# Performance work log

Measured on AMD Instinct MI355X. Metric: run time of the kernel, lower is better.

The kernel has to match this reference:

```python
import jax, jax.numpy as jnp
import numpy as np

E, HID, T, B, NH, DFF, A, C = 116, 64, 512, 64, 4, 2048, 116, 90


def _ln(x, g, b, eps=1e-5):
    m = x.mean(-1, keepdims=True)
    v = ((x - m) ** 2).mean(-1, keepdims=True)
    return (x - m) / jnp.sqrt(v + eps) * g + b


def _layer(x, p):
    # torch TransformerEncoderLayer, post-norm, relu, eval mode (no dropout)
    wqkv, bqkv, wo, bo, g1, bn1, w1, b1, w2, b2, g2, bn2 = p
    S, N, Em = x.shape  # note: S is the attended axis (dim 0), N the batched axis
    dh = Em // NH
    qkv = x @ wqkv.T + bqkv
    q, k, v = jnp.split(qkv, 3, axis=-1)
    q = q.reshape(S, N, NH, dh)
    k = k.reshape(S, N, NH, dh)
    v = v.reshape(S, N, NH, dh)
    scores = jnp.einsum('snhd,tnhd->nhst', q, k) / np.float32(np.sqrt(dh))
    attn = jax.nn.softmax(scores, axis=-1)
    o = jnp.einsum('nhst,tnhd->snhd', attn, v).reshape(S, N, Em)
    o = o @ wo.T + bo
    x = _ln(x + o, g1, bn1)
    f = jax.nn.relu(x @ w1.T + b1) @ w2.T + b2
    return _ln(x + f, g2, bn2)


def _forward(x, sim, p1, p2, fc_w, fc_b):
    out = _layer(x, p1)
    out1 = _layer(out, p2)
    outs = jnp.transpose(out1, (0, 2, 1))       # (B, E, T)
    fea_ = outs @ fc_w.T + fc_b                 # (B, E, HID)
    feas = jnp.transpose(fea_, (0, 2, 1))       # (B, HID, E)
    fea = feas[:, None, :, :, None]             # (B,1,HID,E,1)
    sim32 = sim.astype(jnp.float32)             # (A, HID, C)
    # cosine_similarity over the HID axis (dim=2 of broadcast tensors),
    # computed without materializing the (B,A,HID,E,C) broadcast product.
    dot = jnp.einsum('bhd,ahc->badc', feas, sim32)           # (B,A,E,C)
    fn = jnp.linalg.norm(feas, axis=1)                       # (B,E)
    sn = jnp.linalg.norm(sim32, axis=1)                      # (A,C)
    denom = jnp.maximum(fn[:, None, :, None] * sn[None, :, None, :], 1e-8)
    similarity = dot / denom                                 # (B,A,E,C)
    similar = similarity.reshape(-1, 116 * 90)
    nrm = jnp.maximum(jnp.linalg.norm(similar, axis=1, keepdims=True), 1e-12)
    similar = similar / nrm
    return fea, similarity, similar


_PNAMES = ['wqkv', 'bqkv', 'wo', 'bo', 'g1', 'bn1', 'w1', 'b1', 'w2', 'b2', 'g2', 'bn2']
_PSHAPES = [(3 * E, E), (3 * E,), (E, E), (E,), (E,), (E,), (DFF, E), (DFF,), (E, DFF), (E,), (E,), (E,)]


def setup_inputs() -> dict:
    key = jax.random.key(0)
    ks = jax.random.split(key, 32)
    s = 0.02
    inp = {
        'x': jax.random.normal(ks[0], (B, T, E), jnp.float32),
        'sim': jax.random.normal(ks[1], (A, HID, C), jnp.float32),
    }
    i = 2
    for L in ('l1', 'l2'):
        for nm, sh in zip(_PNAMES, _PSHAPES):
            if nm in ('g1', 'g2'):
                inp[f'{L}_{nm}'] = jnp.ones(sh, jnp.float32)
            elif nm in ('bqkv', 'bo', 'bn1', 'b1', 'b2', 'bn2'):
                inp[f'{L}_{nm}'] = jnp.zeros(sh, jnp.float32)
            else:
                inp[f'{L}_{nm}'] = jax.random.normal(ks[i], sh, jnp.float32) * s
                i += 1
    inp['fc_w'] = jax.random.normal(ks[i], (HID, T), jnp.float32) * s
    inp['fc_b'] = jnp.zeros((HID,), jnp.float32)
    return inp


def reference(x, sim,
              l1_wqkv, l1_bqkv, l1_wo, l1_bo, l1_g1, l1_bn1, l1_w1, l1_b1, l1_w2, l1_b2, l1_g2, l1_bn2,
              l2_wqkv, l2_bqkv, l2_wo, l2_bo, l2_g1, l2_bn1, l2_w1, l2_b1, l2_w2, l2_b2, l2_g2, l2_bn2,
              fc_w, fc_b):
    p1 = (l1_wqkv, l1_bqkv, l1_wo, l1_bo, l1_g1, l1_bn1, l1_w1, l1_b1, l1_w2, l1_b2, l1_g2, l1_bn2)
    p2 = (l2_wqkv, l2_bqkv, l2_wo, l2_bo, l2_g1, l2_bn1, l2_w1, l2_b1, l2_w2, l2_b2, l2_g2, l2_bn2)
    return _forward(x, sim, p1, p2, fc_w, fc_b)
```

## Files before the change

kernel.cpp:

```cpp
#include <hip/hip_runtime.h>
#include <hip/hip_bf16.h>

typedef __attribute__((ext_vector_type(8))) short short8v;
typedef __attribute__((ext_vector_type(4))) float floatx4;
typedef unsigned short ushort_t;

__device__ __forceinline__ float bf2f(unsigned short u) {
  union { unsigned int i; float f; } c;
  c.i = ((unsigned int)u) << 16;
  return c.f;
}
__device__ __forceinline__ unsigned short f2bf(float f) {
  __hip_bfloat16 h = __float2bfloat16(f);
  return *reinterpret_cast<unsigned short*>(&h);
}

struct ConvJobs {
  const float* src[9];
  unsigned short* dst[9];
  int K[9];
  int Kp[9];
  int mode[9];
  int cum[10];
};

__global__ __launch_bounds__(256) void convert_all_kernel(ConvJobs J) {
  const int total = J.cum[9];
  for (int idx = blockIdx.x * 256 + threadIdx.x; idx < total;
       idx += gridDim.x * 256) {
    int j = 0;
    while (idx >= J.cum[j + 1]) ++j;
    const int local = idx - J.cum[j];
    const int Kp = J.Kp[j];
    const int r = local / Kp, c = local - r * Kp;
    unsigned short v;
    if (J.mode[j] == 0) {
      v = (c < J.K[j]) ? f2bf(J.src[j][(size_t)r * J.K[j] + c])
                       : (unsigned short)0;
    } else {
      const int h = c >> 5, d = c & 31;
      v = (d < 29) ? f2bf(J.src[j][(size_t)r * 116 + h * 29 + d])
                   : (unsigned short)0;
    }
    J.dst[j][local] = v;
  }
}

template <int MODE>
__global__ __launch_bounds__(256) void mgemm_kernel(
    const unsigned short* __restrict__ A, const unsigned short* __restrict__ B,
    const float* __restrict__ bias, int N, int Kp, int ldout,
    unsigned short* __restrict__ Yb) {
  __shared__ __align__(16) unsigned short As[128][64];
  __shared__ __align__(16) unsigned short Bs[128][64];

  const int tid = threadIdx.x;
  const int M0 = blockIdx.x * 128;
  const int N0 = blockIdx.y * 128;
  const int wid = tid >> 6, lane = tid & 63;
  const int wr = wid >> 1, wc = wid & 1;
  const int lc = lane & 15, g = lane >> 4;
  const int srow = tid >> 1, shalf = tid & 1;
  const int sw = srow & 7;

  floatx4 acc[4][4] = {};

  const int nk = Kp >> 6;
  for (int kt = 0; kt < nk; ++kt) {
    const int k0 = kt << 6;
    {
      const uint4* p = reinterpret_cast<const uint4*>(
          A + (size_t)(M0 + srow) * Kp + k0 + shalf * 32);
      uint4 v0 = p[0], v1 = p[1], v2 = p[2], v3 = p[3];
      *reinterpret_cast<uint4*>(&As[srow][((((shalf << 2) | 0) ^ sw) << 3)]) = v0;
      *reinterpret_cast<uint4*>(&As[srow][((((shalf << 2) | 1) ^ sw) << 3)]) = v1;
      *reinterpret_cast<uint4*>(&As[srow][((((shalf << 2) | 2) ^ sw) << 3)]) = v2;
      *reinterpret_cast<uint4*>(&As[srow][((((shalf << 2) | 3) ^ sw) << 3)]) = v3;
    }
    {
      uint4 v0 = {0, 0, 0, 0}, v1 = v0, v2 = v0, v3 = v0;
      const int jr = N0 + srow;
      if (jr < N) {
        const uint4* p = reinterpret_cast<const uint4*>(
            B + (size_t)jr * Kp + k0 + shalf * 32);
        v0 = p[0]; v1 = p[1]; v2 = p[2]; v3 = p[3];
      }
      *reinterpret_cast<uint4*>(&Bs[srow][((((shalf << 2) | 0) ^ sw) << 3)]) = v0;
      *reinterpret_cast<uint4*>(&Bs[srow][((((shalf << 2) | 1) ^ sw) << 3)]) = v1;
      *reinterpret_cast<uint4*>(&Bs[srow][((((shalf << 2) | 2) ^ sw) << 3)]) = v2;
      *reinterpret_cast<uint4*>(&Bs[srow][((((shalf << 2) | 3) ^ sw) << 3)]) = v3;
    }
    __syncthreads();
#pragma unroll
    for (int ks = 0; ks < 2; ++ks) {
      short8v a[4], b[4];
#pragma unroll
      for (int m = 0; m < 4; ++m) {
        const int row = wr * 64 + m * 16 + lc;
        a[m] = *reinterpret_cast<const short8v*>(
            &As[row][((((ks << 2) | g) ^ (lc & 7)) << 3)]);
      }
#pragma unroll
      for (int n = 0; n < 4; ++n) {
        const int col = wc * 64 + n * 16 + lc;
        b[n] = *reinterpret_cast<const short8v*>(
            &Bs[col][((((ks << 2) | g) ^ (lc & 7)) << 3)]);
      }
#pragma unroll
      for (int m = 0; m < 4; ++m)
#pragma unroll
        for (int n = 0; n < 4; ++n)
          acc[m][n] = __builtin_amdgcn_mfma_f32_16x16x32_bf16(a[m], b[n],
                                                              acc[m][n], 0, 0, 0);
    }
    __syncthreads();
  }

#pragma unroll
  for (int m = 0; m < 4; ++m) {
#pragma unroll
    for (int r = 0; r < 4; ++r) {
      const int row = M0 + wr * 64 + m * 16 + g * 4 + r;
#pragma unroll
      for (int n = 0; n < 4; ++n) {
        const int col = N0 + wc * 64 + n * 16 + lc;
        if (col < N) {
          float v = acc[m][n][r] + bias[col];
          if (MODE == 1) v = fmaxf(v, 0.f);
          if constexpr (MODE == 3) {
            const int which = (col >= 232) ? 2 : (col >= 116 ? 1 : 0);
            const int cw = col - which * 116;
            const int h = (cw * 565) >> 14;
            const int d = cw - h * 29;
            const int nn2 = row & 511, ss = row >> 9;
            Yb[(size_t)which * 4194304 +
               ((((size_t)nn2 * 4 + h) * 64 + ss) << 5) + d] = f2bf(v);
          } else {
            Yb[(size_t)row * ldout + col] = f2bf(v);
          }
        }
      }
    }
  }
}

__global__ __launch_bounds__(256) void mgemm64_ln_kernel(
    const unsigned short* __restrict__ A, const unsigned short* __restrict__ B,
    const float* __restrict__ bias, int Kp, unsigned short* __restrict__ Yb,
    float* __restrict__ Yf, const float* __restrict__ res,
    const float* __restrict__ gw, const float* __restrict__ bw) {
  __shared__ __align__(16) unsigned short As[64][64];
  __shared__ __align__(16) unsigned short Bs[128][64];
  __shared__ float sum1[2][64];
  __shared__ float sum2[2][64];

  const int tid = threadIdx.x;
  const int M0 = blockIdx.x * 64;
  const int wid = tid >> 6, lane = tid & 63;
  const int wr = wid >> 1, wc = wid & 1;
  const int lc = lane & 15, g = lane >> 4;
  const int arow = tid >> 2, aq = tid & 3;
  const int brow = tid >> 1, bhalf = tid & 1;

  floatx4 acc[2][4] = {};

  const int nk = Kp >> 6;
  for (int kt = 0; kt < nk; ++kt) {
    const int k0 = kt << 6;
    {
      const uint4* p = reinterpret_cast<const uint4*>(
          A + (size_t)(M0 + arow) * Kp + k0 + aq * 16);
      uint4 v0 = p[0], v1 = p[1];
      const int swa = arow & 7;
      *reinterpret_cast<uint4*>(&As[arow][(((aq * 2) ^ swa) << 3)]) = v0;
      *reinterpret_cast<uint4*>(&As[arow][(((aq * 2 + 1) ^ swa) << 3)]) = v1;
    }
    {
      uint4 v0 = {0, 0, 0, 0}, v1 = v0, v2 = v0, v3 = v0;
      if (brow < 116) {
        const uint4* p = reinterpret_cast<const uint4*>(
            B + (size_t)brow * Kp + k0 + bhalf * 32);
        v0 = p[0]; v1 = p[1]; v2 = p[2]; v3 = p[3];
      }
      const int sw = brow & 7;
      *reinterpret_cast<uint4*>(&Bs[brow][((((bhalf << 2) | 0) ^ sw) << 3)]) = v0;
      *reinterpret_cast<uint4*>(&Bs[brow][((((bhalf << 2) | 1) ^ sw) << 3)]) = v1;
      *reinterpret_cast<uint4*>(&Bs[brow][((((bhalf << 2) | 2) ^ sw) << 3)]) = v2;
      *reinterpret_cast<uint4*>(&Bs[brow][((((bhalf << 2) | 3) ^ sw) << 3)]) = v3;
    }
    __syncthreads();
#pragma unroll
    for (int ks = 0; ks < 2; ++ks) {
      short8v a[2], b[4];
#pragma unroll
      for (int m = 0; m < 2; ++m) {
        const int row = wr * 32 + m * 16 + lc;
        a[m] = *reinterpret_cast<const short8v*>(
            &As[row][((((ks << 2) | g) ^ (row & 7)) << 3)]);
      }
#pragma unroll
      for (int n = 0; n < 4; ++n) {
        const int col = wc * 64 + n * 16 + lc;
        b[n] = *reinterpret_cast<const short8v*>(
            &Bs[col][((((ks << 2) | g) ^ (col & 7)) << 3)]);
      }
#pragma unroll
      for (int m = 0; m < 2; ++m)
#pragma unroll
        for (int n = 0; n < 4; ++n)
          acc[m][n] = __builtin_amdgcn_mfma_f32_16x16x32_bf16(a[m], b[n],
                                                              acc[m][n], 0, 0, 0);
    }
    __syncthreads();
  }

  float s1l[2][4], s2l[2][4];
#pragma unroll
  for (int m = 0; m < 2; ++m) {
#pragma unroll
    for (int r = 0; r < 4; ++r) {
      const int row = M0 + wr * 32 + m * 16 + g * 4 + r;
      float s = 0.f, s2 = 0.f;
#pragma unroll
      for (int n = 0; n < 4; ++n) {
        const int col = wc * 64 + n * 16 + lc;
        float v = 0.f;
        if (col < 116)
          v = acc[m][n][r] + bias[col] + res[(size_t)row * 116 + col];
        acc[m][n][r] = v;
        s += v;
        s2 = fmaf(v, v, s2);
      }
#pragma unroll
      for (int st = 1; st < 16; st <<= 1) {
        s += __shfl_xor(s, st, 16);
        s2 += __shfl_xor(s2, st, 16);
      }
      s1l[m][r] = s;
      s2l[m][r] = s2;
    }
  }
  if (lc == 0) {
#pragma unroll
    for (int m = 0; m < 2; ++m)
#pragma unroll
      for (int r = 0; r < 4; ++r) {
        const int lrow = wr * 32 + m * 16 + g * 4 + r;
        sum1[wc][lrow] = s1l[m][r];
        sum2[wc][lrow] = s2l[m][r];
      }
  }
  __syncthreads();
#pragma unroll
  for (int m = 0; m < 2; ++m) {
#pragma unroll
    for (int r = 0; r < 4; ++r) {
      const int lrow = wr * 32 + m * 16 + g * 4 + r;
      const int row = M0 + lrow;
      const float st = sum1[0][lrow] + sum1[1][lrow];
      const float s2t = sum2[0][lrow] + sum2[1][lrow];
      const float mean = st * (1.f / 116.f);
      const float var = s2t * (1.f / 116.f) - mean * mean;
      const float rstd = 1.f / sqrtf(var + 1e-5f);
#pragma unroll
      for (int n = 0; n < 4; ++n) {
        const int col = wc * 64 + n * 16 + lc;
        if (col < 116) {
          const float y = (acc[m][n][r] - mean) * rstd * gw[col] + bw[col];
          Yf[(size_t)row * 116 + col] = y;
          Yb[(size_t)row * 128 + col] = f2bf(y);
        } else {
          Yb[(size_t)row * 128 + col] = 0;
        }
      }
    }
  }
}

__global__ __launch_bounds__(64) void attn_kernel(
    const unsigned short* __restrict__ qkvp, unsigned short* __restrict__ obuf) {
  const int h = blockIdx.x & 3;
  const int n = blockIdx.x >> 2;
  const int s = threadIdx.x;
  __shared__ float ks[64][36];
  __shared__ float vs[64][36];

  const size_t rb = (((size_t)n * 4 + h) * 64 + s) * 32;
  const uint4* qp = reinterpret_cast<const uint4*>(qkvp + rb);
  const uint4* kp = reinterpret_cast<const uint4*>(qkvp + 4194304 + rb);
  const uint4* vp = reinterpret_cast<const uint4*>(qkvp + 8388608 + rb);
  uint4 qv[4], kv4[4], vv4[4];
#pragma unroll
  for (int i = 0; i < 4; ++i) {
    qv[i] = qp[i];
    kv4[i] = kp[i];
    vv4[i] = vp[i];
  }
  float q[32], kf[32], vf[32];
#pragma unroll
  for (int i = 0; i < 4; ++i) {
    const unsigned* wq = reinterpret_cast<const unsigned*>(&qv[i]);
    const unsigned* wk = reinterpret_cast<const unsigned*>(&kv4[i]);
    const unsigned* wv = reinterpret_cast<const unsigned*>(&vv4[i]);
#pragma unroll
    for (int j = 0; j < 4; ++j) {
      union { unsigned u; float f; } lo, hi;
      const int d0 = i * 8 + 2 * j;
      lo.u = wq[j] << 16; hi.u = wq[j] & 0xffff0000u;
      q[d0] = lo.f; q[d0 + 1] = hi.f;
      lo.u = wk[j] << 16; hi.u = wk[j] & 0xffff0000u;
      kf[d0] = (d0 < 29) ? lo.f : 0.f;
      kf[d0 + 1] = (d0 + 1 < 29) ? hi.f : 0.f;
      lo.u = wv[j] << 16; hi.u = wv[j] & 0xffff0000u;
      vf[d0] = (d0 < 29) ? lo.f : 0.f;
      vf[d0 + 1] = (d0 + 1 < 29) ? hi.f : 0.f;
    }
  }
  q[29] = q[30] = q[31] = 0.f;
#pragma unroll
  for (int c = 0; c < 8; ++c) {
    *reinterpret_cast<float4*>(&ks[s][c * 4]) =
        make_float4(kf[4 * c], kf[4 * c + 1], kf[4 * c + 2], kf[4 * c + 3]);
    *reinterpret_cast<float4*>(&vs[s][c * 4]) =
        make_float4(vf[4 * c], vf[4 * c + 1], vf[4 * c + 2], vf[4 * c + 3]);
  }
  __syncthreads();

  const float scale = 0.18569533817705186f;
  float sc[64];
#pragma unroll 4
  for (int t = 0; t < 64; ++t) {
    const float4* kr = reinterpret_cast<const float4*>(&ks[t][0]);
    float a = 0.f;
#pragma unroll
    for (int c = 0; c < 8; ++c) {
      const float4 kc = kr[c];
      a = fmaf(q[4 * c], kc.x, a);
      a = fmaf(q[4 * c + 1], kc.y, a);
      a = fmaf(q[4 * c + 2], kc.z, a);
      a = fmaf(q[4 * c + 3], kc.w, a);
    }
    sc[t] = a * scale;
  }
  float m = sc[0];
#pragma unroll
  for (int t = 1; t < 64; ++t) m = fmaxf(m, sc[t]);
  float sum = 0.f;
#pragma unroll
  for (int t = 0; t < 64; ++t) {
    sc[t] = __expf(sc[t] - m);
    sum += sc[t];
  }
  const float inv = 1.f / sum;
  float o[32] = {};
#pragma unroll 4
  for (int t = 0; t < 64; ++t) {
    const float p = sc[t];
    const float4* vr = reinterpret_cast<const float4*>(&vs[t][0]);
#pragma unroll
    for (int c = 0; c < 8; ++c) {
      const float4 vc = vr[c];
      o[4 * c] = fmaf(p, vc.x, o[4 * c]);
      o[4 * c + 1] = fmaf(p, vc.y, o[4 * c + 1]);
      o[4 * c + 2] = fmaf(p, vc.z, o[4 * c + 2]);
      o[4 * c + 3] = fmaf(p, vc.w, o[4 * c + 3]);
    }
  }
  unsigned short ow[32];
#pragma unroll
  for (int i = 0; i < 32; ++i) ow[i] = f2bf(o[i] * inv);
  uint4* od =
      reinterpret_cast<uint4*>(obuf + ((size_t)s * 512 + n) * 128 + h * 32);
  const uint4* ows = reinterpret_cast<const uint4*>(ow);
#pragma unroll
  for (int i = 0; i < 4; ++i) od[i] = ows[i];
}

__global__ __launch_bounds__(256) void fc_kernel(const float* __restrict__ X4,
                                                 const float* __restrict__ fw,
                                                 const float* __restrict__ fb,
                                                 float* __restrict__ fea) {
  const int eg = blockIdx.x;
  const int b = blockIdx.y;
  const int e0 = eg * 29;
  __shared__ float Os[64][30];
  __shared__ float Wf[64][65];
  const int tid = threadIdx.x;
  const int h = tid & 63, jg = tid >> 6;
  float acc[8] = {};

  for (int tc = 0; tc < 8; ++tc) {
    for (int idx = tid; idx < 64 * 29; idx += 256) {
      int tt = idx / 29;
      int ee = idx - tt * 29;
      Os[tt][ee] = X4[((size_t)b * 512 + tc * 64 + tt) * 116 + e0 + ee];
    }
    for (int idx = tid; idx < 64 * 64; idx += 256) {
      int hh = idx >> 6, t2 = idx & 63;
      Wf[hh][t2] = fw[(size_t)hh * 512 + tc * 64 + t2];
    }
    __syncthreads();
#pragma unroll 4
    for (int t = 0; t < 64; ++t) {
      const float w = Wf[h][t];
#pragma unroll
      for (int m = 0; m < 8; ++m) {
        const int el = jg + 4 * m;
        if (el < 29) acc[m] = fmaf(Os[t][el], w, acc[m]);
      }
    }
    __syncthreads();
  }
  const float bb = fb[h];
#pragma unroll
  for (int m = 0; m < 8; ++m) {
    const int el = jg + 4 * m;
    if (el < 29) fea[((size_t)b * 64 + h) * 116 + e0 + el] = acc[m] + bb;
  }
}

__global__ __launch_bounds__(256) void sim_prep_kernel(
    const float* __restrict__ fea, const float* __restrict__ simin,
    unsigned short* __restrict__ feaT, unsigned short* __restrict__ simT,
    float* __restrict__ fn, float* __restrict__ sn) {
  __shared__ float L[64][121];
  const int blk = blockIdx.x;
  const int tid = threadIdx.x;
  if (blk < 64) {
    const int b = blk;
    for (int idx = tid; idx < 64 * 116; idx += 256) {
      const int h = idx / 116, d = idx - h * 116;
      L[h][d] = bf2f(f2bf(fea[((size_t)b * 64 + h) * 116 + d]));
    }
    __syncthreads();
    for (int idx = tid; idx < 128 * 64; idx += 256) {
      const int d = idx >> 6, h = idx & 63;
      feaT[((size_t)b * 128 + d) * 64 + h] = (d < 116) ? f2bf(L[h][d]) : 0;
    }
    if (tid < 116) {
      float s = 0.f;
#pragma unroll 8
      for (int h = 0; h < 64; ++h) {
        const float t = L[h][tid];
        s = fmaf(t, t, s);
      }
      fn[b * 128 + tid] = sqrtf(s);
    }
  } else {
    const int a = blk - 64;
    for (int idx = tid; idx < 64 * 90; idx += 256) {
      const int h = idx / 90, c = idx - h * 90;
      L[h][c] = bf2f(f2bf(simin[((size_t)a * 64 + h) * 90 + c]));
    }
    __syncthreads();
    for (int idx = tid; idx < 96 * 64; idx += 256) {
      const int c = idx >> 6, h = idx & 63;
      simT[((size_t)a * 96 + c) * 64 + h] = (c < 90) ? f2bf(L[h][c]) : 0;
    }
    if (tid < 90) {
      float s = 0.f;
#pragma unroll 8
      for (int h = 0; h < 64; ++h) {
        const float t = L[h][tid];
        s = fmaf(t, t, s);
      }
      sn[a * 96 + tid] = sqrtf(s);
    }
  }
}

__global__ __launch_bounds__(256) void sim_mfma2_kernel(
    const unsigned short* __restrict__ feaT, const unsigned short* __restrict__ simT,
    const float* __restrict__ fn, const float* __restrict__ sn,
    float* __restrict__ simil, float* __restrict__ similar) {
  const int a = blockIdx.x;
  const int b = blockIdx.y;
  __shared__ __align__(16) unsigned char shmem[41760];
  __shared__ float fnrow[116];
  __shared__ float snrow[90];
  __shared__ float wred[4];
  const int tid = threadIdx.x;

  unsigned short (*Ft)[64] = reinterpret_cast<unsigned short(*)[64]>(shmem);
  unsigned short (*St)[64] =
      reinterpret_cast<unsigned short(*)[64]>(shmem + 16384);
  float* Rs = reinterpret_cast<float*>(shmem);

  const int srow = tid >> 1, shalf = tid & 1;
  const int sw = srow & 7;
  {
    const uint4* p = reinterpret_cast<const uint4*>(
        feaT + ((size_t)b * 128 + srow) * 64 + shalf * 32);
    uint4 v0 = p[0], v1 = p[1], v2 = p[2], v3 = p[3];
    *reinterpret_cast<uint4*>(&Ft[srow][((((shalf << 2) | 0) ^ sw) << 3)]) = v0;
    *reinterpret_cast<uint4*>(&Ft[srow][((((shalf << 2) | 1) ^ sw) << 3)]) = v1;
    *reinterpret_cast<uint4*>(&Ft[srow][((((shalf << 2) | 2) ^ sw) << 3)]) = v2;
    *reinterpret_cast<uint4*>(&Ft[srow][((((shalf << 2) | 3) ^ sw) << 3)]) = v3;
  }
  if (srow < 96) {
    const uint4* p = reinterpret_cast<const uint4*>(
        simT + ((size_t)a * 96 + srow) * 64 + shalf * 32);
    uint4 v0 = p[0], v1 = p[1], v2 = p[2], v3 = p[3];
    *reinterpret_cast<uint4*>(&St[srow][((((shalf << 2) | 0) ^ sw) << 3)]) = v0;
    *reinterpret_cast<uint4*>(&St[srow][((((shalf << 2) | 1) ^ sw) << 3)]) = v1;
    *reinterpret_cast<uint4*>(&St[srow][((((shalf << 2) | 2) ^ sw) << 3)]) = v2;
    *reinterpret_cast<uint4*>(&St[srow][((((shalf << 2) | 3) ^ sw) << 3)]) = v3;
  }
  if (tid < 116) fnrow[tid] = fn[b * 128 + tid];
  else if (tid >= 128 && tid < 218) snrow[tid - 128] = sn[a * 96 + tid - 128];
  __syncthreads();

  const int wid = tid >> 6, lane = tid & 63;
  const int wr = wid >> 1, wc = wid & 1;
  const int lc = lane & 15, g = lane >> 4;

  floatx4 acc[4][3] = {};
#pragma unroll
  for (int ks = 0; ks < 2; ++ks) {
    short8v av[4], bv[3];
#pragma unroll
    for (int m = 0; m < 4; ++m) {
      const int row = wr * 64 + m * 16 + lc;
      av[m] = *reinterpret_cast<const short8v*>(
          &Ft[row][((((ks << 2) | g) ^ (lc & 7)) << 3)]);
    }
#pragma unroll
    for (int n = 0; n < 3; ++n) {
      const int col = wc * 48 + n * 16 + lc;
      bv[n] = *reinterpret_cast<const short8v*>(
          &St[col][((((ks << 2) | g) ^ (lc & 7)) << 3)]);
    }
#pragma unroll
    for (int m = 0; m < 4; ++m)
#pragma unroll
      for (int n = 0; n < 3; ++n)
        acc[m][n] = __builtin_amdgcn_mfma_f32_16x16x32_bf16(av[m], bv[n],
                                                            acc[m][n], 0, 0, 0);
  }
  __syncthreads();

  float ss = 0.f;
#pragma unroll
  for (int m = 0; m < 4; ++m) {
#pragma unroll
    for (int r = 0; r < 4; ++r) {
      const int d = wr * 64 + m * 16 + g * 4 + r;
      if (d < 116) {
        const float fnv = fnrow[d];
#pragma unroll
        for (int n = 0; n < 3; ++n) {
          const int c = wc * 48 + n * 16 + lc;
          if (c < 90) {
            const float denom = fmaxf(fnv * snrow[c], 1e-8f);
            float rcp = __builtin_amdgcn_rcpf(denom);
            rcp = rcp * (2.0f - denom * rcp);
            const float v = acc[m][n][r] * rcp;
            ss = fmaf(v, v, ss);
            Rs[d * 90 + c] = v;
          }
        }
      }
    }
  }
#pragma unroll
  for (int st = 1; st <= 32; st <<= 1) ss += __shfl_xor(ss, st, 64);
  if (lane == 0) wred[wid] = ss;
  __syncthreads();
  const float tot = wred[0] + wred[1] + wred[2] + wred[3];
  const float inv = 1.f / fmaxf(sqrtf(tot), 1e-12f);

  const size_t rowbase = ((size_t)b * 116 + a) * (116 * 90);
  float4* so = reinterpret_cast<float4*>(simil + rowbase);
  float4* sr = reinterpret_cast<float4*>(similar + rowbase);
  const float4* rs4 = reinterpret_cast<const float4*>(Rs);
  for (int i = tid; i < 2610; i += 256) {
    float4 v = rs4[i];
    so[i] = v;
    float4 w;
    w.x = v.x * inv; w.y = v.y * inv; w.z = v.z * inv; w.w = v.w * inv;
    sr[i] = w;
  }
}

__global__ __launch_bounds__(256) void sim_mfma_kernel(
    const float* __restrict__ fea, const float* __restrict__ simin,
    float* __restrict__ simil, float* __restrict__ similar) {
  const int a = blockIdx.x;
  const int b = blockIdx.y;
  __shared__ __align__(16) unsigned char shmem[41760];
  __shared__ float fnrow[116];
  __shared__ float snrow[90];
  __shared__ float wred[4];
  const int tid = threadIdx.x;

  unsigned short (*Ft)[64] = reinterpret_cast<unsigned short(*)[64]>(shmem);
  unsigned short (*St)[64] =
      reinterpret_cast<unsigned short(*)[64]>(shmem + 16384);
  float* Rs = reinterpret_cast<float*>(shmem);

  for (int idx = tid; idx < 64 * 116; idx += 256) {
    const int h = idx / 116, d = idx - h * 116;
    Ft[d][(((h >> 3) ^ (d & 7)) << 3) | (h & 7)] =
        f2bf(fea[((size_t)b * 64 + h) * 116 + d]);
  }
  for (int idx = tid; idx < 12 * 64; idx += 256) {
    const int d = 116 + (idx >> 6), h = idx & 63;
    Ft[d][(((h >> 3) ^ (d & 7)) << 3) | (h & 7)] = 0;
  }
  for (int idx = tid; idx < 64 * 90; idx += 256) {
    const int h = idx / 90, c = idx - h * 90;
    St[c][(((h >> 3) ^ (c & 7)) << 3) | (h & 7)] =
        f2bf(simin[((size_t)a * 64 + h) * 90 + c]);
  }
  for (int idx = tid; idx < 6 * 64; idx += 256) {
    const int c = 90 + (idx >> 6), h = idx & 63;
    St[c][(((h >> 3) ^ (c & 7)) << 3) | (h & 7)] = 0;
  }
  __syncthreads();

  if (tid < 116) {
    float s = 0.f;
#pragma unroll 8
    for (int h = 0; h < 64; ++h) {
      const float t = bf2f(Ft[tid][(((h >> 3) ^ (tid & 7)) << 3) | (h & 7)]);
      s = fmaf(t, t, s);
    }
    fnrow[tid] = sqrtf(s);
  } else if (tid >= 128 && tid < 218) {
    const int c = tid - 128;
    float s = 0.f;
#pragma unroll 8
    for (int h = 0; h < 64; ++h) {
      const float t = bf2f(St[c][(((h >> 3) ^ (c & 7)) << 3) | (h & 7)]);
      s = fmaf(t, t, s);
    }
    snrow[c] = sqrtf(s);
  }
  __syncthreads();

  const int wid = tid >> 6, lane = tid & 63;
  const int wr = wid >> 1, wc = wid & 1;
  const int lc = lane & 15, g = lane >> 4;

  floatx4 acc[4][3] = {};
#pragma unroll
  for (int ks = 0; ks < 2; ++ks) {
    short8v av[4], bv[3];
#pragma unroll
    for (int m = 0; m < 4; ++m) {
      const int row = wr * 64 + m * 16 + lc;
      av[m] = *reinterpret_cast<const short8v*>(
          &Ft[row][((((ks << 2) | g) ^ (lc & 7)) << 3)]);
    }
#pragma unroll
    for (int n = 0; n < 3; ++n) {
      const int col = wc * 48 + n * 16 + lc;
      bv[n] = *reinterpret_cast<const short8v*>(
          &St[col][((((ks << 2) | g) ^ (lc & 7)) << 3)]);
    }
#pragma unroll
    for (int m = 0; m < 4; ++m)
#pragma unroll
      for (int n = 0; n < 3; ++n)
        acc[m][n] = __builtin_amdgcn_mfma_f32_16x16x32_bf16(av[m], bv[n],
                                                            acc[m][n], 0, 0, 0);
  }
  __syncthreads();

  float ss = 0.f;
#pragma unroll
  for (int m = 0; m < 4; ++m) {
#pragma unroll
    for (int r = 0; r < 4; ++r) {
      const int d = wr * 64 + m * 16 + g * 4 + r;
      if (d < 116) {
        const float fnv = fnrow[d];
#pragma unroll
        for (int n = 0; n < 3; ++n) {
          const int c = wc * 48 + n * 16 + lc;
          if (c < 90) {
            const float denom = fmaxf(fnv * snrow[c], 1e-8f);
            float rcp = __builtin_amdgcn_rcpf(denom);
            rcp = rcp * (2.0f - denom * rcp);
            const float v = acc[m][n][r] * rcp;
            ss = fmaf(v, v, ss);
            Rs[d * 90 + c] = v;
          }
        }
      }
    }
  }
#pragma unroll
  for (int st = 1; st <= 32; st <<= 1) ss += __shfl_xor(ss, st, 64);
  if (lane == 0) wred[wid] = ss;
  __syncthreads();
  const float tot = wred[0] + wred[1] + wred[2] + wred[3];
  const float inv = 1.f / fmaxf(sqrtf(tot), 1e-12f);

  const size_t rowbase = ((size_t)b * 116 + a) * (116 * 90);
  float4* so = reinterpret_cast<float4*>(simil + rowbase);
  float4* sr = reinterpret_cast<float4*>(similar + rowbase);
  const float4* rs4 = reinterpret_cast<const float4*>(Rs);
  for (int i = tid; i < 2610; i += 256) {
    float4 v = rs4[i];
    so[i] = v;
    float4 w;
    w.x = v.x * inv; w.y = v.y * inv; w.z = v.z * inv; w.w = v.w * inv;
    sr[i] = w;
  }
}

extern "C" void kernel_launch(void* const* d_in, const int* in_sizes, int n_in,
                              void* d_out, int out_size, void* d_ws,
                              size_t ws_size, hipStream_t stream) {
  const float* x0 = (const float*)d_in[0];
  const float* simin = (const float*)d_in[1];
  const float* p[24];
  for (int i = 0; i < 24; ++i) p[i] = (const float*)d_in[2 + i];
  const float* fc_w = (const float*)d_in[26];
  const float* fc_b = (const float*)d_in[27];

  float* out = (float*)d_out;
  float* fea = out;
  float* simil = out + 475136;
  float* similar = out + 77981696;

  float* xa_f[2] = {similar + 0, similar + 7602176};
  float* xb_f[2] = {similar + 3801088, similar + 11403264};
  unsigned short* obufb = (unsigned short*)(similar + 15204352);
  unsigned short* qkvp = (unsigned short*)(similar + 17301504);
  unsigned short* Ab = (unsigned short*)(similar + 23592960);
  unsigned short* xab[2] = {(unsigned short*)(similar + 25690112),
                            (unsigned short*)(similar + 29884416)};
  unsigned short* xbb[2] = {(unsigned short*)(similar + 27787264),
                            (unsigned short*)(similar + 31981568)};
  unsigned short* hbufb = (unsigned short*)simil;
  unsigned short* wbuf = (unsigned short*)(simil + 33554432);
  const size_t WSZ = 559104;

  unsigned char* ws = (unsigned char*)d_ws;
  unsigned short* feaT = (unsigned short*)ws;
  unsigned short* simT = (unsigned short*)(ws + 1048576);
  float* fnb = (float*)(ws + 2473984);
  float* snb = (float*)(ws + 2506752);
  const bool ws_ok = ws_size >= 2551296;

  {
    ConvJobs J;
    int cum = 0;
    auto add = [&](int j, const float* s, unsigned short* dd, int R, int K,
                   int Kp, int mode) {
      J.src[j] = s; J.dst[j] = dd; J.K[j] = K; J.Kp[j] = Kp; J.mode[j] = mode;
      J.cum[j] = cum; cum += R * Kp;
    };
    add(0, x0, Ab, 32768, 116, 128, 0);
    for (int L = 0; L < 2; ++L) {
      unsigned short* wb = wbuf + L * WSZ;
      add(1 + L * 4, p[L * 12 + 0], wb + 0, 348, 116, 128, 0);
      add(2 + L * 4, p[L * 12 + 2], wb + 44544, 116, 116, 128, 1);
      add(3 + L * 4, p[L * 12 + 6], wb + 59392, 2048, 116, 128, 0);
      add(4 + L * 4, p[L * 12 + 8], wb + 321536, 116, 2048, 2048, 0);
    }
    J.cum[9] = cum;
    hipLaunchKernelGGL(convert_all_kernel, dim3(2048), dim3(256), 0, stream, J);
  }

  const unsigned short* Ain = Ab;
  const float* resin = x0;
  for (int L = 0; L < 2; ++L) {
    unsigned short* wb = wbuf + L * WSZ;
    const float* bqkv = p[L * 12 + 1];
    const float* bo = p[L * 12 + 3];
    const float* g1 = p[L * 12 + 4];
    const float* bn1 = p[L * 12 + 5];
    const float* b1 = p[L * 12 + 7];
    const float* b2 = p[L * 12 + 9];
    const float* g2 = p[L * 12 + 10];
    const float* bn2 = p[L * 12 + 11];

    hipLaunchKernelGGL((mgemm_kernel<3>), dim3(256, 3), dim3(256), 0, stream,
                       Ain, wb + 0, bqkv, 348, 128, 0, qkvp);
    hipLaunchKernelGGL(attn_kernel, dim3(2048), dim3(64), 0, stream, qkvp,
                       obufb);
    hipLaunchKernelGGL(mgemm64_ln_kernel, dim3(512), dim3(256), 0, stream,
                       obufb, wb + 44544, bo, 128, xab[L], xa_f[L], resin, g1,
                       bn1);
    hipLaunchKernelGGL((mgemm_kernel<1>), dim3(256, 16), dim3(256), 0, stream,
                       xab[L], wb + 59392, b1, 2048, 128, 2048, hbufb);
    hipLaunchKernelGGL(mgemm64_ln_kernel, dim3(512), dim3(256), 0, stream,
                       hbufb, wb + 321536, b2, 2048, xbb[L], xb_f[L], xa_f[L],
                       g2, bn2);
    Ain = xbb[L];
    resin = xb_f[L];
  }

  hipLaunchKernelGGL(fc_kernel, dim3(4, 64), dim3(256), 0, stream, xb_f[1],
                     fc_w, fc_b, fea);
  if (ws_ok) {
    hipLaunchKernelGGL(sim_prep_kernel, dim3(180), dim3(256), 0, stream, fea,
                       simin, feaT, simT, fnb, snb);
    hipLaunchKernelGGL(sim_mfma2_kernel, dim3(116, 64), dim3(256), 0, stream,
                       feaT, simT, fnb, snb, simil, similar);
  } else {
    hipLaunchKernelGGL(sim_mfma_kernel, dim3(116, 64), dim3(256), 0, stream,
                       fea, simin, simil, similar);
  }
}
```

Measured before the change: 754.5 us.

## Fuse FFN up-projection, ReLU, down-projection and LayerNorm into one kernel

Replaces the separate W1 GEMM (writing a bf16 hidden buffer to global memory) and the W2+LayerNorm GEMM with a single kernel. Each block processes 64 tokens, computes the hidden activations in 64-wide chunks into shared memory, and immediately accumulates the down-projection. This removes the large global hidden-buffer round trip and one launch per layer. In exchange, every block re-streams the full W1/W2 weights, and the chunk loop synchronizes three times per iteration without load/compute overlap.

Result: faster. 662.8 us (-12.2%).

```diff
diff --git a/kernel.cpp b/kernel.cpp
--- a/kernel.cpp
+++ b/kernel.cpp
@@ -3,7 +3,6 @@
 
 typedef __attribute__((ext_vector_type(8))) short short8v;
 typedef __attribute__((ext_vector_type(4))) float floatx4;
-typedef unsigned short ushort_t;
 
 __device__ __forceinline__ float bf2f(unsigned short u) {
   union { unsigned int i; float f; } c;
@@ -277,6 +276,203 @@
   }
 }
 
+__global__ __launch_bounds__(256) void ffn_fused_kernel(
+    const unsigned short* __restrict__ Xa,
+    const unsigned short* __restrict__ W1,
+    const float* __restrict__ b1,
+    const unsigned short* __restrict__ W2,
+    const float* __restrict__ b2, const float* __restrict__ res,
+    const float* __restrict__ gw, const float* __restrict__ bw,
+    unsigned short* __restrict__ Yb,
+    float* __restrict__ Yf) {
+  __shared__ __align__(16) unsigned short Xs[64][128];
+  __shared__ __align__(16) unsigned short W1c[64][128];
+  __shared__ __align__(16) unsigned short W2c[128][64];
+  __shared__ __align__(16) unsigned short Hs[64][64];
+  __shared__ float sum1[2][64];
+  __shared__ float sum2[2][64];
+
+  const int tid = threadIdx.x;
+  const int M0 = blockIdx.x * 64;
+  const int wid = tid >> 6, lane = tid & 63;
+  const int wr = wid >> 1, wc = wid & 1;
+  const int lc = lane & 15, g = lane >> 4;
+  const int arow = tid >> 2, aq = tid & 3;
+  const int brow = tid >> 1, bh = tid & 1;
+
+  {
+    const uint4* p = reinterpret_cast<const uint4*>(
+        Xa + (size_t)(M0 + arow) * 128 + aq * 32);
+#pragma unroll
+    for (int q = 0; q < 4; ++q) {
+      const int cj = aq * 4 + q;
+      const int swz = (cj & 8) | ((cj ^ arow) & 7);
+      *reinterpret_cast<uint4*>(&Xs[arow][swz * 8]) = p[q];
+    }
+  }
+
+  floatx4 oacc[2][4] = {};
+
+  for (int kc = 0; kc < 32; ++kc) {
+    {
+      const uint4* p = reinterpret_cast<const uint4*>(
+          W1 + (size_t)(kc * 64 + arow) * 128 + aq * 32);
+#pragma unroll
+      for (int q = 0; q < 4; ++q) {
+        const int cj = aq * 4 + q;
+        const int swz = (cj & 8) | ((cj ^ arow) & 7);
+        *reinterpret_cast<uint4*>(&W1c[arow][swz * 8]) = p[q];
+      }
+    }
+    {
+      uint4 v[4] = {};
+      if (brow < 116) {
+        const uint4* p = reinterpret_cast<const uint4*>(
+            W2 + (size_t)brow * 2048 + kc * 64 + bh * 32);
+        v[0] = p[0]; v[1] = p[1]; v[2] = p[2]; v[3] = p[3];
+      }
+#pragma unroll
+      for (int q = 0; q < 4; ++q) {
+        const int cj = bh * 4 + q;
+        const int swz = (cj ^ brow) & 7;
+        *reinterpret_cast<uint4*>(&W2c[brow][swz * 8]) = v[q];
+      }
+    }
+    __syncthreads();
+
+    floatx4 hacc[2][2] = {};
+#pragma unroll
+    for (int ks = 0; ks < 4; ++ks) {
+      short8v av[2], bv[2];
+#pragma unroll
+      for (int m = 0; m < 2; ++m) {
+        const int row = wr * 32 + m * 16 + lc;
+        const int cj = ks * 4 + g;
+        const int swz = (cj & 8) | ((cj ^ row) & 7);
+        av[m] = *reinterpret_cast<const short8v*>(&Xs[row][swz * 8]);
+      }
+#pragma unroll
+      for (int n = 0; n < 2; ++n) {
+        const int row = wc * 32 + n * 16 + lc;
+        const int cj = ks * 4 + g;
+        const int swz = (cj & 8) | ((cj ^ row) & 7);
+        bv[n] = *reinterpret_cast<const short8v*>(&W1c[row][swz * 8]);
+      }
+#pragma unroll
+      for (int m = 0; m < 2; ++m)
+#pragma unroll
+        for (int n = 0; n < 2; ++n)
+          hacc[m][n] = __builtin_amdgcn_mfma_f32_16x16x32_bf16(av[m], bv[n],
+                                                               hacc[m][n], 0, 0, 0);
+    }
+#pragma unroll
+    for (int n = 0; n < 2; ++n) {
+      const int dff = wc * 32 + n * 16 + lc;
+      const float bb = b1[kc * 64 + dff];
+      const int cj = dff >> 3;
+      const int dlo = dff & 7;
+#pragma unroll
+      for (int m = 0; m < 2; ++m) {
+#pragma unroll
+        for (int r = 0; r < 4; ++r) {
+          const int tok = wr * 32 + m * 16 + g * 4 + r;
+          const float hv = fmaxf(hacc[m][n][r] + bb, 0.f);
+          Hs[tok][(((cj ^ tok) & 7) << 3) | dlo] = f2bf(hv);
+        }
+      }
+    }
+    __syncthreads();
+
+#pragma unroll
+    for (int ks = 0; ks < 2; ++ks) {
+      short8v av[2], bv[4];
+#pragma unroll
+      for (int m = 0; m < 2; ++m) {
+        const int row = wr * 32 + m * 16 + lc;
+        const int cj = ks * 4 + g;
+        av[m] = *reinterpret_cast<const short8v*>(
+            &Hs[row][(((cj ^ row) & 7) << 3)]);
+      }
+#pragma unroll
+      for (int n = 0; n < 4; ++n) {
+        const int col = wc * 64 + n * 16 + lc;
+        const int cj = ks * 4 + g;
+        bv[n] = *reinterpret_cast<const short8v*>(
+            &W2c[col][(((cj ^ col) & 7) << 3)]);
+      }
+#pragma unroll
+      for (int m = 0; m < 2; ++m)
+#pragma unroll
+        for (int n = 0; n < 4; ++n)
+          oacc[m][n] = __builtin_amdgcn_mfma_f32_16x16x32_bf16(av[m], bv[n],
+                                                               oacc[m][n], 0, 0, 0);
+    }
+    __syncthreads();
+  }
+
+  float s1l[2][4], s2l[2][4];
+#pragma unroll
+  for (int m = 0; m < 2; ++m) {
+#pragma unroll
+    for (int r = 0; r < 4; ++r) {
+      const int row = M0 + wr * 32 + m * 16 + g * 4 + r;
+      float s = 0.f, s2 = 0.f;
+#pragma unroll
+      for (int n = 0; n < 4; ++n) {
+        const int col = wc * 64 + n * 16 + lc;
+        float v = 0.f;
+        if (col < 116)
+          v = oacc[m][n][r] + b2[col] + res[(size_t)row * 116 + col];
+        oacc[m][n][r] = v;
+        s += v;
+        s2 = fmaf(v, v, s2);
+      }
+#pragma unroll
+      for (int st = 1; st < 16; st <<= 1) {
+        s += __shfl_xor(s, st, 16);
+        s2 += __shfl_xor(s2, st, 16);
+      }
+      s1l[m][r] = s;
+      s2l[m][r] = s2;
+    }
+  }
+  if (lc == 0) {
+#pragma unroll
+    for (int m = 0; m < 2; ++m)
+#pragma unroll
+      for (int r = 0; r < 4; ++r) {
+        const int lrow = wr * 32 + m * 16 + g * 4 + r;
+        sum1[wc][lrow] = s1l[m][r];
+        sum2[wc][lrow] = s2l[m][r];
+      }
+  }
+  __syncthreads();
+#pragma unroll
+  for (int m = 0; m < 2; ++m) {
+#pragma unroll
+    for (int r = 0; r < 4; ++r) {
+      const int lrow = wr * 32 + m * 16 + g * 4 + r;
+      const int row = M0 + lrow;
+      const float st = sum1[0][lrow] + sum1[1][lrow];
+      const float s2t = sum2[0][lrow] + sum2[1][lrow];
+      const float mean = st * (1.f / 116.f);
+      const float var = s2t * (1.f / 116.f) - mean * mean;
+      const float rstd = 1.f / sqrtf(var + 1e-5f);
+#pragma unroll
+      for (int n = 0; n < 4; ++n) {
+        const int col = wc * 64 + n * 16 + lc;
+        if (col < 116) {
+          const float y = (oacc[m][n][r] - mean) * rstd * gw[col] + bw[col];
+          Yf[(size_t)row * 116 + col] = y;
+          Yb[(size_t)row * 128 + col] = f2bf(y);
+        } else {
+          Yb[(size_t)row * 128 + col] = 0;
+        }
+      }
+    }
+  }
+}
+
 __global__ __launch_bounds__(64) void attn_kernel(
     const unsigned short* __restrict__ qkvp, unsigned short* __restrict__ obuf) {
   const int h = blockIdx.x & 3;
@@ -734,7 +930,6 @@
                             (unsigned short*)(similar + 29884416)};
   unsigned short* xbb[2] = {(unsigned short*)(similar + 27787264),
                             (unsigned short*)(similar + 31981568)};
-  unsigned short* hbufb = (unsigned short*)simil;
   unsigned short* wbuf = (unsigned short*)(simil + 33554432);
   const size_t WSZ = 559104;
 
@@ -785,11 +980,9 @@
     hipLaunchKernelGGL(mgemm64_ln_kernel, dim3(512), dim3(256), 0, stream,
                        obufb, wb + 44544, bo, 128, xab[L], xa_f[L], resin, g1,
                        bn1);
-    hipLaunchKernelGGL((mgemm_kernel<1>), dim3(256, 16), dim3(256), 0, stream,
-                       xab[L], wb + 59392, b1, 2048, 128, 2048, hbufb);
-    hipLaunchKernelGGL(mgemm64_ln_kernel, dim3(512), dim3(256), 0, stream,
-                       hbufb, wb + 321536, b2, 2048, xbb[L], xb_f[L], xa_f[L],
-                       g2, bn2);
+    hipLaunchKernelGGL(ffn_fused_kernel, dim3(512), dim3(256), 0, stream,
+                       xab[L], wb + 59392, b1, wb + 321536, b2, xa_f[L], g2,
+                       bn2, xbb[L], xb_f[L]);
     Ain = xbb[L];
     resin = xb_f[L];
   }
```
